# Kernel tuning notes

Hardware: AMD Instinct MI355X
Metric: run time of the kernel (lower is better)

## Reference

```python
import jax, jax.numpy as jnp
import numpy as np

DIM = 2048
N_HEADS = 32
N_KV_HEADS = 8
HEAD_DIM = 64
REPEATS = N_HEADS // N_KV_HEADS
SCALE = HEAD_DIM ** -0.5
L = 2048
B = 1


def rotary_matrix(context_len, d):
    # Dense (L, d, d) RoPE rotation matrix, exactly as get_rotary_matrix1.
    pos = jnp.arange(1, context_len + 1, dtype=jnp.float32)[:, None]
    i = jnp.arange(d // 2)
    theta = 10000.0 ** (-2.0 * i.astype(jnp.float32) / d)
    m_theta = pos * theta  # (L, d/2)
    cos_v, sin_v = jnp.cos(m_theta), jnp.sin(m_theta)
    R = jnp.zeros((context_len, d, d), dtype=jnp.float32)
    R = R.at[:, 2 * i, 2 * i].set(cos_v)
    R = R.at[:, 2 * i, 2 * i + 1].set(-sin_v)
    R = R.at[:, 2 * i + 1, 2 * i].set(sin_v)
    R = R.at[:, 2 * i + 1, 2 * i + 1].set(cos_v)
    return R


def causal_mask(context_len):
    idx = jnp.arange(context_len)
    return (idx[:, None] < idx[None, :]).astype(jnp.float32) * -1e9


def setup_inputs() -> dict:
    key = jax.random.key(0)
    ks = jax.random.split(key, 5)
    x = jax.random.normal(ks[0], (B, L, DIM), dtype=jnp.float32)
    mask = causal_mask(L)
    wq_w = jax.random.normal(ks[1], (N_HEADS * HEAD_DIM, DIM), dtype=jnp.float32) * 0.02
    wk_w = jax.random.normal(ks[2], (N_KV_HEADS * HEAD_DIM, DIM), dtype=jnp.float32) * 0.02
    wv_w = jax.random.normal(ks[3], (N_KV_HEADS * HEAD_DIM, DIM), dtype=jnp.float32) * 0.02
    wo_w = jax.random.normal(ks[4], (DIM, N_HEADS * HEAD_DIM), dtype=jnp.float32) * 0.02
    return {"x": x, "mask": mask, "wq_w": wq_w, "wk_w": wk_w, "wv_w": wv_w, "wo_w": wo_w}


def reference(x, mask, wq_w, wk_w, wv_w, wo_w):
    Bx, Lx, D = x.shape
    # projections (torch Linear: y = x @ W.T)
    q = jnp.einsum('bld,od->blo', x, wq_w).reshape(Bx, Lx, N_HEADS, HEAD_DIM).transpose(0, 2, 1, 3)
    k = jnp.einsum('bld,od->blo', x, wk_w).reshape(Bx, Lx, N_KV_HEADS, HEAD_DIM).transpose(0, 2, 1, 3)
    v = jnp.einsum('bld,od->blo', x, wv_w).reshape(Bx, Lx, N_KV_HEADS, HEAD_DIM).transpose(0, 2, 1, 3)
    # GQA repeat of kv heads (interleaved, matching concat-unsqueeze-reshape)
    k = jnp.repeat(k, REPEATS, axis=1)
    v = jnp.repeat(v, REPEATS, axis=1)
    # dense-matrix RoPE on q and (repeated) k
    R = rotary_matrix(Lx, HEAD_DIM)
    q = jnp.einsum('bhlj,lij->bhli', q, R)
    k = jnp.einsum('bhlj,lij->bhli', k, R)
    scores = jnp.einsum('bhld,bhmd->bhlm', q, k) * SCALE + mask
    attn = jax.nn.softmax(scores.astype(jnp.float32), axis=-1)
    out = jnp.einsum('bhlm,bhmd->bhld', attn, v)
    out = out.transpose(0, 2, 1, 3).reshape(Bx, Lx, N_HEADS * HEAD_DIM)
    out = jnp.einsum('blo,do->bld', out, wo_w)
    return out, k, v
```

## Files before the change

kernel.cpp:

```cpp
#include <hip/hip_runtime.h>

typedef __bf16 bf16;
typedef __bf16 bf16x8 __attribute__((ext_vector_type(8)));
typedef float floatx4 __attribute__((ext_vector_type(4)));
typedef float floatx16 __attribute__((ext_vector_type(16)));
typedef unsigned int uint;

#define MFMA16(a, b, c) __builtin_amdgcn_mfma_f32_16x16x32_bf16((a), (b), (c), 0, 0, 0)
#define MFMA32(a, b, c) __builtin_amdgcn_mfma_f32_32x32x16_bf16((a), (b), (c), 0, 0, 0)

__device__ __forceinline__ void gl2lds16(const bf16* g, bf16* l) {
  __builtin_amdgcn_global_load_lds(
      (const __attribute__((address_space(1))) void*)g,
      (__attribute__((address_space(3))) void*)l, 16, 0, 0);
}
__device__ __forceinline__ void wait_vm0() { __builtin_amdgcn_s_waitcnt(0x0f70); }

__device__ __forceinline__ void cvt8(const float* __restrict__ s,
                                     bf16* __restrict__ d, int i8) {
  const float4 a = ((const float4*)s)[i8 * 2];
  const float4 b = ((const float4*)s)[i8 * 2 + 1];
  bf16x8 o;
  o[0] = (bf16)a.x; o[1] = (bf16)a.y; o[2] = (bf16)a.z; o[3] = (bf16)a.w;
  o[4] = (bf16)b.x; o[5] = (bf16)b.y; o[6] = (bf16)b.z; o[7] = (bf16)b.w;
  *(bf16x8*)(d + i8 * 8) = o;
}

__global__ __launch_bounds__(256) void convert_kernel(
    const float* __restrict__ x, const float* __restrict__ wq,
    const float* __restrict__ wk, const float* __restrict__ wv,
    const float* __restrict__ wo, bf16* __restrict__ xb,
    bf16* __restrict__ wqb, bf16* __restrict__ wkb, bf16* __restrict__ wvb,
    bf16* __restrict__ wob) {
  const int g = blockIdx.x * 256 + threadIdx.x;
  if (g < 524288) cvt8(x, xb, g);
  else if (g < 1048576) cvt8(wq, wqb, g - 524288);
  else if (g < 1179648) cvt8(wk, wkb, g - 1048576);
  else if (g < 1310720) cvt8(wv, wvb, g - 1179648);
  else cvt8(wo, wob, g - 1310720);
}

template <typename OutT>
__device__ __forceinline__ void gemm_tile_body64(
    const bf16* __restrict__ A, int lda,
    const bf16* __restrict__ B, int ldb,
    OutT* __restrict__ C, int ldc, int K,
    bf16* S) {
  const int t = threadIdx.x;
  const int w = t >> 6, lane = t & 63;
  const int l15 = lane & 15, qd = lane >> 4;
  const int wr = w >> 1, wc = w & 1;

  floatx4 acc[2][4];
#pragma unroll
  for (int i = 0; i < 2; ++i)
#pragma unroll
    for (int j = 0; j < 4; ++j) acc[i][j] = (floatx4){0.f, 0.f, 0.f, 0.f};

  const bf16* gb[6];
  int lo[6];
#pragma unroll
  for (int i = 0; i < 6; ++i) {
    const int u = w + 4 * i;
    lo[i] = u * 512 + lane * 8;
    if (u < 8) {
      gb[i] = A + ((u >> 1) * 16 + l15) * lda + (u & 1) * 32 + qd * 8;
    } else {
      const int v = u - 8;
      gb[i] = B + ((v >> 1) * 16 + l15) * ldb + (v & 1) * 32 + qd * 8;
    }
  }

#define STG64(kt_, buf_)                                            \
  {                                                                 \
    bf16* d_ = S + (buf_) * 12288;                                  \
    _Pragma("unroll")                                               \
    for (int i_ = 0; i_ < 6; ++i_)                                  \
      gl2lds16(gb[i_] + (kt_) * 64, d_ + lo[i_]);                   \
  }

  const int NT = K >> 6;
  STG64(0, 0);
  wait_vm0();
  __syncthreads();
  int cur = 0;
  for (int kt = 0; kt < NT; ++kt) {
    if (kt + 1 < NT) STG64(kt + 1, cur ^ 1);
    const bf16* Ab = S + cur * 12288;
    const bf16* Bb = Ab + 4096;
    bf16x8 a[2][2], b[4][2];
#pragma unroll
    for (int i = 0; i < 2; ++i)
#pragma unroll
      for (int kk = 0; kk < 2; ++kk)
        a[i][kk] =
            *(const bf16x8*)(Ab + ((wr * 2 + i) * 2 + kk) * 512 + lane * 8);
#pragma unroll
    for (int j = 0; j < 4; ++j)
#pragma unroll
      for (int kk = 0; kk < 2; ++kk)
        b[j][kk] =
            *(const bf16x8*)(Bb + ((wc * 4 + j) * 2 + kk) * 512 + lane * 8);
#pragma unroll
    for (int kk = 0; kk < 2; ++kk)
#pragma unroll
      for (int i = 0; i < 2; ++i)
#pragma unroll
        for (int j = 0; j < 4; ++j)
          acc[i][j] = MFMA16(a[i][kk], b[j][kk], acc[i][j]);
    wait_vm0();
    __builtin_amdgcn_sched_barrier(0);
    __builtin_amdgcn_s_barrier();
    __builtin_amdgcn_sched_barrier(0);
    cur ^= 1;
  }
#undef STG64

#pragma unroll
  for (int i = 0; i < 2; ++i)
#pragma unroll
    for (int j = 0; j < 4; ++j) {
      const int row = wr * 32 + i * 16 + qd * 4;
      const int col = wc * 64 + j * 16 + l15;
#pragma unroll
      for (int r = 0; r < 4; ++r)
        C[(row + r) * ldc + col] = (OutT)acc[i][j][r];
    }
}

__global__ __launch_bounds__(256) void gemm_qkv(
    const bf16* __restrict__ x, const bf16* __restrict__ wq,
    const bf16* __restrict__ wk, const bf16* __restrict__ wv,
    bf16* __restrict__ Qws, bf16* __restrict__ Kh, bf16* __restrict__ Vh,
    bf16* __restrict__ Vt) {
  __shared__ bf16 As[4096], Bs[4096];
  const int bid = blockIdx.y * 24 + blockIdx.x;
  const int swz = (bid & 7) * 48 + (bid >> 3);
  const int nb = swz % 24;
  const int m0 = (swz / 24) * 128;
  const bf16* B;
  if (nb < 16) B = wq + nb * 128 * 2048;
  else if (nb < 20) B = wk + (nb - 16) * 128 * 2048;
  else B = wv + (nb - 20) * 128 * 2048;

  const int t = threadIdx.x;
  const int w = t >> 6, lane = t & 63;
  const int l15 = lane & 15, qd = lane >> 4;
  const int wr = w >> 1, wc = w & 1;

  floatx4 acc[4][4];
#pragma unroll
  for (int i = 0; i < 4; ++i)
#pragma unroll
    for (int j = 0; j < 4; ++j) acc[i][j] = (floatx4){0.f, 0.f, 0.f, 0.f};

  const bf16* A = x + m0 * 2048;
  const int mt0 = w, mt1 = w + 4;
  const int kseg = qd * 8;
  const bf16* ga0 = A + (mt0 * 16 + l15) * 2048 + kseg;
  const bf16* ga1 = A + (mt1 * 16 + l15) * 2048 + kseg;
  const bf16* gb0 = B + (mt0 * 16 + l15) * 2048 + kseg;
  const bf16* gb1 = B + (mt1 * 16 + l15) * 2048 + kseg;
  bf16* lA0 = As + mt0 * 512 + lane * 8;
  bf16* lA1 = As + mt1 * 512 + lane * 8;
  bf16* lB0 = Bs + mt0 * 512 + lane * 8;
  bf16* lB1 = Bs + mt1 * 512 + lane * 8;

  for (int k0 = 0; k0 < 2048; k0 += 32) {
    gl2lds16(ga0 + k0, lA0);
    gl2lds16(ga1 + k0, lA1);
    gl2lds16(gb0 + k0, lB0);
    gl2lds16(gb1 + k0, lB1);
    wait_vm0();
    __syncthreads();

    bf16x8 a[4], b[4];
#pragma unroll
    for (int i = 0; i < 4; ++i)
      a[i] = *(const bf16x8*)(As + (wr * 4 + i) * 512 + lane * 8);
#pragma unroll
    for (int j = 0; j < 4; ++j)
      b[j] = *(const bf16x8*)(Bs + (wc * 4 + j) * 512 + lane * 8);
#pragma unroll
    for (int i = 0; i < 4; ++i)
#pragma unroll
      for (int j = 0; j < 4; ++j) acc[i][j] = MFMA16(a[i], b[j], acc[i][j]);
    __syncthreads();
  }

  const float NEG_LOG2_10000_D32 = -0.4152410118609203f;
  const int odd = l15 & 1;
#pragma unroll
  for (int i = 0; i < 4; ++i)
#pragma unroll
    for (int j = 0; j < 4; ++j) {
      const int row = wr * 64 + i * 16 + qd * 4;
      const int col = wc * 64 + j * 16 + l15;
#pragma unroll
      for (int r = 0; r < 4; ++r) {
        const float own = acc[i][j][r];
        const int rg = m0 + row + r;
        if (nb < 16) {
          const float part = __shfl_xor(own, 1);
          const int gcol = nb * 128 + col;
          const int a = (gcol & 63) >> 1;
          const float ang =
              (float)(rg + 1) * exp2f(NEG_LOG2_10000_D32 * (float)a);
          float s, c;
          __sincosf(ang, &s, &c);
          const float val = odd ? (s * part + c * own) : (c * own - s * part);
          Qws[rg * 2048 + gcol] = (bf16)val;
        } else if (nb < 20) {
          const float part = __shfl_xor(own, 1);
          const int g512 = (nb - 16) * 128 + col;
          const int kvh = g512 >> 6, d = g512 & 63;
          const int a = d >> 1;
          const float ang =
              (float)(rg + 1) * exp2f(NEG_LOG2_10000_D32 * (float)a);
          float s, c;
          __sincosf(ang, &s, &c);
          const float val = odd ? (s * part + c * own) : (c * own - s * part);
          Kh[(kvh * 2048 + rg) * 64 + d] = (bf16)val;
        } else {
          const int g512 = (nb - 20) * 128 + col;
          const int kvh = g512 >> 6, d = g512 & 63;
          Vh[(kvh * 2048 + rg) * 64 + d] = (bf16)own;
          Vt[kvh * 131072 + d * 2048 + rg] = (bf16)own;
        }
      }
    }
}

__global__ __launch_bounds__(256) void gemm_o(
    const bf16* __restrict__ Ows, const bf16* __restrict__ wo,
    float* __restrict__ out) {
  __shared__ bf16 S[24576];
  const int bid = blockIdx.y * 16 + blockIdx.x;
  const int swz = (bid & 7) * 64 + (bid >> 3);
  const int n0 = (swz & 15) * 128;
  const int m0 = (swz >> 4) * 64;
  gemm_tile_body64<float>(Ows + m0 * 2048, 2048, wo + n0 * 2048, 2048,
                          out + m0 * 2048 + n0, 2048, 2048, S);
}

__global__ __launch_bounds__(256) void flash_kernel(
    const bf16* __restrict__ Qws, const bf16* __restrict__ Kh,
    const bf16* __restrict__ Vh, const bf16* __restrict__ Vt,
    bf16* __restrict__ Ows, float* __restrict__ Opart, float* __restrict__ ML,
    float* __restrict__ kout, float* __restrict__ vout) {
  __shared__ bf16 KVs[2][2][4096];
  __shared__ bf16 Osh[128 * 66];

  const int h = blockIdx.y;
  const int bx = blockIdx.x;
  int qt, seg, kts, kte;
  if (bx < 8) {
    qt = bx; seg = -1; kts = 0; kte = 2 * qt + 2;
  } else {
    const int i = bx - 8;
    qt = 8 + (i >> 1);
    seg = i & 1;
    const int half = qt + 1;
    kts = seg * half;
    kte = kts + half;
  }
  const int kh = h >> 2;
  const int q0 = qt * 128;
  const int t = threadIdx.x, w = t >> 6, lane = t & 63;
  const int l31 = lane & 31, hf = lane >> 5;
  const int qw = q0 + w * 32;

  const int s0 = w, s1 = w + 4;
  const bf16* gK0 = Kh + kh * 131072 + ((s0 >> 2) * 32 + l31) * 64 + (s0 & 3) * 16 + hf * 8;
  const bf16* gK1 = Kh + kh * 131072 + ((s1 >> 2) * 32 + l31) * 64 + (s1 & 3) * 16 + hf * 8;
  const bf16* gV0 = Vt + kh * 131072 + ((s0 >> 2) * 32 + l31) * 2048 + (s0 & 3) * 16 + hf * 8;
  const bf16* gV1 = Vt + kh * 131072 + ((s1 >> 2) * 32 + l31) * 2048 + (s1 & 3) * 16 + hf * 8;

  {
    const int nb = kts & 1;
    gl2lds16(gK0 + kts * 4096, &KVs[nb][0][s0 * 512 + lane * 8]);
    gl2lds16(gK1 + kts * 4096, &KVs[nb][0][s1 * 512 + lane * 8]);
    gl2lds16(gV0 + kts * 64, &KVs[nb][1][s0 * 512 + lane * 8]);
    gl2lds16(gV1 + kts * 64, &KVs[nb][1][s1 * 512 + lane * 8]);
  }

  bf16x8 qf[4];
  {
    const bf16* qrow = Qws + (qw + l31) * 2048 + h * 64 + hf * 8;
#pragma unroll
    for (int c = 0; c < 4; ++c) qf[c] = *(const bf16x8*)(qrow + c * 16);
  }

  {
    const int bid = (int)blockIdx.y * 24 + (int)blockIdx.x;
    for (uint u = (uint)(bid * 256 + t); u < 262144u; u += 196608u) {
      const uint u2 = u & 131071u;
      const bf16* src = (u < 131072u) ? Kh : Vh;
      float* dst = (u < 131072u) ? kout : vout;
      const int kvh2 = u2 >> 14;
      const int rr = u2 & 16383;
      const int l = rr >> 3, d8 = (rr & 7) * 8;
      const bf16x8 v = *(const bf16x8*)(src + (kvh2 * 2048 + l) * 64 + d8);
      float4 f0, f1;
      f0.x = (float)v[0]; f0.y = (float)v[1]; f0.z = (float)v[2]; f0.w = (float)v[3];
      f1.x = (float)v[4]; f1.y = (float)v[5]; f1.z = (float)v[6]; f1.w = (float)v[7];
#pragma unroll
      for (int rep = 0; rep < 4; ++rep) {
        float* o2 = dst + (((kvh2 * 4 + rep) * 2048 + l) * 64 + d8);
        *(float4*)o2 = f0;
        *(float4*)(o2 + 4) = f1;
      }
    }
  }

  floatx16 o[2] = {};
  float mrun = -3e38f, lrun = 0.f;

  const float C = 0.1803368801f;
  for (int kt = kts; kt < kte; ++kt) {
    wait_vm0();
    __syncthreads();
    if (kt + 1 < kte) {
      const int nb = (kt + 1) & 1;
      const int koff = (kt + 1) * 4096, voff = (kt + 1) * 64;
      gl2lds16(gK0 + koff, &KVs[nb][0][s0 * 512 + lane * 8]);
      gl2lds16(gK1 + koff, &KVs[nb][0][s1 * 512 + lane * 8]);
      gl2lds16(gV0 + voff, &KVs[nb][1][s0 * 512 + lane * 8]);
      gl2lds16(gV1 + voff, &KVs[nb][1][s1 * 512 + lane * 8]);
    }
    const int kt64 = kt * 64;
    if (kt64 > qw + 31) continue;
    const bf16* Kb = &KVs[kt & 1][0][0];
    const bf16* Vb = &KVs[kt & 1][1][0];

    floatx16 st[2];
    __builtin_amdgcn_s_setprio(1);
#pragma unroll
    for (int tt = 0; tt < 2; ++tt) {
      floatx16 z = {};
#pragma unroll
      for (int c = 0; c < 4; ++c) {
        const bf16x8 kf = *(const bf16x8*)(Kb + (tt * 4 + c) * 512 + lane * 8);
        z = MFMA32(kf, qf[c], z);
      }
      st[tt] = z;
    }
    __builtin_amdgcn_s_setprio(0);
    if (kt64 + 64 > qw) {
      const int myq = qw + l31;
#pragma unroll
      for (int tt = 0; tt < 2; ++tt)
#pragma unroll
        for (int r = 0; r < 16; ++r) {
          const int key = kt64 + tt * 32 + (r & 3) + 8 * (r >> 2) + 4 * hf;
          if (key > myq) st[tt][r] = -1e30f;
        }
    }
    float ma = -3e38f, mb = -3e38f, mc = -3e38f, md = -3e38f;
#pragma unroll
    for (int tt = 0; tt < 2; ++tt)
#pragma unroll
      for (int r = 0; r < 16; r += 4) {
        ma = fmaxf(ma, st[tt][r + 0]);
        mb = fmaxf(mb, st[tt][r + 1]);
        mc = fmaxf(mc, st[tt][r + 2]);
        md = fmaxf(md, st[tt][r + 3]);
      }
    float mx = fmaxf(fmaxf(ma, mb), fmaxf(mc, md));
    mx = fmaxf(mx, __shfl_xor(mx, 32));
    const bool defer = __all((mx - mrun) * C <= 8.f);
    if (!defer) {
      const float mn = fmaxf(mrun, mx);
      const float al = __builtin_amdgcn_exp2f((mrun - mn) * C);
      lrun *= al;
#pragma unroll
      for (int n = 0; n < 2; ++n)
#pragma unroll
        for (int r = 0; r < 16; ++r) o[n][r] *= al;
      mrun = mn;
    }
    float ra = 0.f, rb = 0.f, rc = 0.f, rd = 0.f;
#pragma unroll
    for (int tt = 0; tt < 2; ++tt)
#pragma unroll
      for (int r = 0; r < 16; r += 4) {
        const float p0 = __builtin_amdgcn_exp2f((st[tt][r + 0] - mrun) * C);
        const float p1 = __builtin_amdgcn_exp2f((st[tt][r + 1] - mrun) * C);
        const float p2 = __builtin_amdgcn_exp2f((st[tt][r + 2] - mrun) * C);
        const float p3 = __builtin_amdgcn_exp2f((st[tt][r + 3] - mrun) * C);
        st[tt][r + 0] = p0; ra += p0;
        st[tt][r + 1] = p1; rb += p1;
        st[tt][r + 2] = p2; rc += p2;
        st[tt][r + 3] = p3; rd += p3;
      }
    float rs = (ra + rb) + (rc + rd);
    rs += __shfl_xor(rs, 32);
    lrun += rs;

    uint pk[2][4][2];
#pragma unroll
    for (int tt = 0; tt < 2; ++tt)
#pragma unroll
      for (int g = 0; g < 4; ++g)
#pragma unroll
        for (int p = 0; p < 2; ++p) {
          union { bf16 h2[2]; uint u; } cv;
          cv.h2[0] = (bf16)st[tt][4 * g + 2 * p];
          cv.h2[1] = (bf16)st[tt][4 * g + 2 * p + 1];
          pk[tt][g][p] = cv.u;
        }
    uint own_[2][2][2], rv[2][2][2];
#pragma unroll
    for (int tt = 0; tt < 2; ++tt)
#pragma unroll
      for (int gam = 0; gam < 2; ++gam)
#pragma unroll
        for (int p = 0; p < 2; ++p) {
          own_[tt][gam][p] = hf ? pk[tt][2 * gam + 1][p] : pk[tt][2 * gam][p];
          const uint snd = hf ? pk[tt][2 * gam][p] : pk[tt][2 * gam + 1][p];
          rv[tt][gam][p] = (uint)__shfl_xor((int)snd, 32);
        }
    __builtin_amdgcn_s_setprio(1);
#pragma unroll
    for (int c = 0; c < 4; ++c) {
      const int tt = c >> 1, gam = c & 1;
      union { uint u[4]; bf16x8 v; } pf;
      pf.u[0] = hf ? rv[tt][gam][0] : own_[tt][gam][0];
      pf.u[1] = hf ? rv[tt][gam][1] : own_[tt][gam][1];
      pf.u[2] = hf ? own_[tt][gam][0] : rv[tt][gam][0];
      pf.u[3] = hf ? own_[tt][gam][1] : rv[tt][gam][1];
#pragma unroll
      for (int n = 0; n < 2; ++n)
        o[n] = MFMA32(*(const bf16x8*)(Vb + (n * 4 + c) * 512 + lane * 8),
                      pf.v, o[n]);
    }
    __builtin_amdgcn_s_setprio(0);
  }

  if (seg < 0) {
    const float inv = 1.f / lrun;
#pragma unroll
    for (int n = 0; n < 2; ++n)
#pragma unroll
      for (int r = 0; r < 16; ++r) {
        const int dl = n * 32 + (r & 3) + 8 * (r >> 2) + 4 * hf;
        Osh[(w * 32 + l31) * 66 + dl] = (bf16)(o[n][r] * inv);
      }
    __syncthreads();
#pragma unroll
    for (int i = 0; i < 4; ++i) {
      const int row = (t >> 3) + i * 32;
      const int col = (t & 7) * 8;
      const bf16x8 vv = *(const bf16x8*)&Osh[row * 66 + col];
      *(bf16x8*)&Ows[(q0 + row) * 2048 + h * 64 + col] = vv;
    }
  } else {
    const int idx = (h * 8 + (qt - 8)) * 2 + seg;
    float* Op = Opart + idx * 8192;
#pragma unroll
    for (int n = 0; n < 2; ++n)
#pragma unroll
      for (int r = 0; r < 16; ++r) {
        const int dl = n * 32 + (r & 3) + 8 * (r >> 2) + 4 * hf;
        Op[dl * 128 + w * 32 + l31] = o[n][r];
      }
    if (hf == 0) {
      ML[idx * 256 + w * 32 + l31] = mrun;
      ML[idx * 256 + 128 + w * 32 + l31] = lrun;
    }
  }
}

__global__ __launch_bounds__(256) void combine_kernel(
    const float* __restrict__ Opart, const float* __restrict__ ML,
    bf16* __restrict__ Ows) {
  __shared__ bf16 Osh[128 * 66];
  const int b = blockIdx.x;
  const int h = b >> 3, qt = (b & 7) + 8;
  const int q0 = qt * 128;
  const int t = threadIdx.x;
  const int row = t & 127, dh = t >> 7;
  const int i0 = (h * 8 + (qt - 8)) * 2;
  const float C = 0.1803368801f;
  const float m0 = ML[i0 * 256 + row], l0 = ML[i0 * 256 + 128 + row];
  const float m1 = ML[(i0 + 1) * 256 + row], l1 = ML[(i0 + 1) * 256 + 128 + row];
  const float m = fmaxf(m0, m1);
  const float w0 = __builtin_amdgcn_exp2f((m0 - m) * C);
  const float w1 = __builtin_amdgcn_exp2f((m1 - m) * C);
  const float inv = 1.f / (l0 * w0 + l1 * w1);
  const float* P0 = Opart + i0 * 8192;
  const float* P1 = Opart + (i0 + 1) * 8192;
#pragma unroll
  for (int j = 0; j < 32; ++j) {
    const int d = dh * 32 + j;
    const float v = (P0[d * 128 + row] * w0 + P1[d * 128 + row] * w1) * inv;
    Osh[row * 66 + d] = (bf16)v;
  }
  __syncthreads();
#pragma unroll
  for (int i = 0; i < 4; ++i) {
    const int r2 = (t >> 3) + i * 32;
    const int col = (t & 7) * 8;
    const bf16x8 vv = *(const bf16x8*)&Osh[r2 * 66 + col];
    *(bf16x8*)&Ows[(q0 + r2) * 2048 + h * 64 + col] = vv;
  }
}

extern "C" void kernel_launch(void* const* d_in, const int* in_sizes, int n_in,
                              void* d_out, int out_size, void* d_ws,
                              size_t ws_size, hipStream_t stream) {
  const float* x = (const float*)d_in[0];
  const float* wq = (const float*)d_in[2];
  const float* wk = (const float*)d_in[3];
  const float* wv = (const float*)d_in[4];
  const float* wo = (const float*)d_in[5];

  float* out = (float*)d_out;
  float* kout = out + 4194304;
  float* vout = out + 8388608;

  bf16* ws = (bf16*)d_ws;
  bf16* xb = ws;
  bf16* wqb = xb + 4194304;
  bf16* wkb = wqb + 4194304;
  bf16* wvb = wkb + 1048576;
  bf16* wob = wvb + 1048576;
  bf16* Qws = wob + 4194304;
  bf16* Kws = Qws + 4194304;
  bf16* Vh = Kws + 1048576;
  bf16* Vt = Vh + 1048576;
  bf16* Ows = Vt + 1048576;
  bf16* Kh = Ows + 4194304;
  float* Opart = out;
  float* MLf = (float*)Kws;

  convert_kernel<<<dim3(7168), dim3(256), 0, stream>>>(x, wq, wk, wv, wo, xb,
                                                       wqb, wkb, wvb, wob);
  gemm_qkv<<<dim3(24, 16), dim3(256), 0, stream>>>(xb, wqb, wkb, wvb, Qws, Kh,
                                                   Vh, Vt);
  flash_kernel<<<dim3(24, 32), dim3(256), 0, stream>>>(Qws, Kh, Vh, Vt, Ows,
                                                       Opart, MLf, kout, vout);
  combine_kernel<<<dim3(256), dim3(256), 0, stream>>>(Opart, MLf, Ows);
  gemm_o<<<dim3(16, 32), dim3(256), 0, stream>>>(Ows, wob, out);
}
```

Baseline: 290.3 us.

## Stage QKV epilogue through LDS for vector stores; load K/V directly in flash

The QKV GEMM epilogue now writes accumulators to a padded LDS tile, then applies RoPE on 8-wide vectors and issues 16-byte coalesced stores. The V transpose to Vt is done from LDS, replacing scattered 2-byte stores. The flash kernel drops its double-buffered LDS staging of K/V and loads fragments straight from global memory into registers per wave. Each wave now stops at its own causal limit, which removes block-wide barriers, but it risks exposed global load latency with no prefetch and redundant global reads across waves.

```diff
diff --git a/kernel.cpp b/kernel.cpp
--- a/kernel.cpp
+++ b/kernel.cpp
@@ -133,7 +133,9 @@
     const bf16* __restrict__ wk, const bf16* __restrict__ wv,
     bf16* __restrict__ Qws, bf16* __restrict__ Kh, bf16* __restrict__ Vh,
     bf16* __restrict__ Vt) {
-  __shared__ bf16 As[4096], Bs[4096];
+  __shared__ bf16 SM[17152];
+  bf16* As = SM;
+  bf16* Bs = SM + 4096;
   const int bid = blockIdx.y * 24 + blockIdx.x;
   const int swz = (bid & 7) * 48 + (bid >> 3);
   const int nb = swz % 24;
@@ -188,8 +190,6 @@
     __syncthreads();
   }
 
-  const float NEG_LOG2_10000_D32 = -0.4152410118609203f;
-  const int odd = l15 & 1;
 #pragma unroll
   for (int i = 0; i < 4; ++i)
 #pragma unroll
@@ -197,38 +197,74 @@
       const int row = wr * 64 + i * 16 + qd * 4;
       const int col = wc * 64 + j * 16 + l15;
 #pragma unroll
-      for (int r = 0; r < 4; ++r) {
-        const float own = acc[i][j][r];
-        const int rg = m0 + row + r;
-        if (nb < 16) {
-          const float part = __shfl_xor(own, 1);
-          const int gcol = nb * 128 + col;
-          const int a = (gcol & 63) >> 1;
-          const float ang =
-              (float)(rg + 1) * exp2f(NEG_LOG2_10000_D32 * (float)a);
-          float s, c;
-          __sincosf(ang, &s, &c);
-          const float val = odd ? (s * part + c * own) : (c * own - s * part);
-          Qws[rg * 2048 + gcol] = (bf16)val;
-        } else if (nb < 20) {
-          const float part = __shfl_xor(own, 1);
-          const int g512 = (nb - 16) * 128 + col;
-          const int kvh = g512 >> 6, d = g512 & 63;
-          const int a = d >> 1;
-          const float ang =
-              (float)(rg + 1) * exp2f(NEG_LOG2_10000_D32 * (float)a);
-          float s, c;
-          __sincosf(ang, &s, &c);
-          const float val = odd ? (s * part + c * own) : (c * own - s * part);
-          Kh[(kvh * 2048 + rg) * 64 + d] = (bf16)val;
-        } else {
-          const int g512 = (nb - 20) * 128 + col;
-          const int kvh = g512 >> 6, d = g512 & 63;
-          Vh[(kvh * 2048 + rg) * 64 + d] = (bf16)own;
-          Vt[kvh * 131072 + d * 2048 + rg] = (bf16)own;
-        }
-      }
-    }
+      for (int r = 0; r < 4; ++r)
+        SM[(row + r) * 134 + col] = (bf16)acc[i][j][r];
+    }
+  __syncthreads();
+
+  const float NEG_LOG2_10000_D32 = -0.4152410118609203f;
+  if (nb < 16) {
+#pragma unroll
+    for (int k = 0; k < 8; ++k) {
+      const int u = t + (k << 8);
+      const int row = u >> 4, c8 = (u & 15) << 3;
+      const bf16x8 v = *(const bf16x8*)&SM[row * 134 + c8];
+      const float base = (float)(m0 + row + 1);
+      bf16x8 ov;
+#pragma unroll
+      for (int p = 0; p < 4; ++p) {
+        const int a = ((c8 & 63) >> 1) + p;
+        float s, c;
+        __sincosf(base * exp2f(NEG_LOG2_10000_D32 * (float)a), &s, &c);
+        const float x0 = (float)v[2 * p], x1 = (float)v[2 * p + 1];
+        ov[2 * p] = (bf16)(c * x0 - s * x1);
+        ov[2 * p + 1] = (bf16)(s * x0 + c * x1);
+      }
+      *(bf16x8*)&Qws[(m0 + row) * 2048 + nb * 128 + c8] = ov;
+    }
+  } else if (nb < 20) {
+#pragma unroll
+    for (int k = 0; k < 8; ++k) {
+      const int u = t + (k << 8);
+      const int row = u >> 4, c8 = (u & 15) << 3;
+      const bf16x8 v = *(const bf16x8*)&SM[row * 134 + c8];
+      const float base = (float)(m0 + row + 1);
+      bf16x8 ov;
+#pragma unroll
+      for (int p = 0; p < 4; ++p) {
+        const int a = ((c8 & 63) >> 1) + p;
+        float s, c;
+        __sincosf(base * exp2f(NEG_LOG2_10000_D32 * (float)a), &s, &c);
+        const float x0 = (float)v[2 * p], x1 = (float)v[2 * p + 1];
+        ov[2 * p] = (bf16)(c * x0 - s * x1);
+        ov[2 * p + 1] = (bf16)(s * x0 + c * x1);
+      }
+      const int g512 = (nb - 16) * 128 + c8;
+      const int kvh = g512 >> 6, d8 = g512 & 63;
+      *(bf16x8*)&Kh[(kvh * 2048 + m0 + row) * 64 + d8] = ov;
+    }
+  } else {
+#pragma unroll
+    for (int k = 0; k < 8; ++k) {
+      const int u = t + (k << 8);
+      const int row = u >> 4, c8 = (u & 15) << 3;
+      const bf16x8 v = *(const bf16x8*)&SM[row * 134 + c8];
+      const int g512 = (nb - 20) * 128 + c8;
+      const int kvh = g512 >> 6, d8 = g512 & 63;
+      *(bf16x8*)&Vh[(kvh * 2048 + m0 + row) * 64 + d8] = v;
+    }
+#pragma unroll
+    for (int k = 0; k < 8; ++k) {
+      const int u = t + (k << 8);
+      const int col = u >> 4, r8 = (u & 15) << 3;
+      bf16x8 v;
+#pragma unroll
+      for (int jj = 0; jj < 8; ++jj) v[jj] = SM[(r8 + jj) * 134 + col];
+      const int g512 = (nb - 20) * 128 + col;
+      const int kvh = g512 >> 6, d = g512 & 63;
+      *(bf16x8*)&Vt[kvh * 131072 + d * 2048 + m0 + r8] = v;
+    }
+  }
 }
 
 __global__ __launch_bounds__(256) void gemm_o(
@@ -248,7 +284,6 @@
     const bf16* __restrict__ Vh, const bf16* __restrict__ Vt,
     bf16* __restrict__ Ows, float* __restrict__ Opart, float* __restrict__ ML,
     float* __restrict__ kout, float* __restrict__ vout) {
-  __shared__ bf16 KVs[2][2][4096];
   __shared__ bf16 Osh[128 * 66];
 
   const int h = blockIdx.y;
@@ -269,27 +304,6 @@
   const int t = threadIdx.x, w = t >> 6, lane = t & 63;
   const int l31 = lane & 31, hf = lane >> 5;
   const int qw = q0 + w * 32;
-
-  const int s0 = w, s1 = w + 4;
-  const bf16* gK0 = Kh + kh * 131072 + ((s0 >> 2) * 32 + l31) * 64 + (s0 & 3) * 16 + hf * 8;
-  const bf16* gK1 = Kh + kh * 131072 + ((s1 >> 2) * 32 + l31) * 64 + (s1 & 3) * 16 + hf * 8;
-  const bf16* gV0 = Vt + kh * 131072 + ((s0 >> 2) * 32 + l31) * 2048 + (s0 & 3) * 16 + hf * 8;
-  const bf16* gV1 = Vt + kh * 131072 + ((s1 >> 2) * 32 + l31) * 2048 + (s1 & 3) * 16 + hf * 8;
-
-  {
-    const int nb = kts & 1;
-    gl2lds16(gK0 + kts * 4096, &KVs[nb][0][s0 * 512 + lane * 8]);
-    gl2lds16(gK1 + kts * 4096, &KVs[nb][0][s1 * 512 + lane * 8]);
-    gl2lds16(gV0 + kts * 64, &KVs[nb][1][s0 * 512 + lane * 8]);
-    gl2lds16(gV1 + kts * 64, &KVs[nb][1][s1 * 512 + lane * 8]);
-  }
-
-  bf16x8 qf[4];
-  {
-    const bf16* qrow = Qws + (qw + l31) * 2048 + h * 64 + hf * 8;
-#pragma unroll
-    for (int c = 0; c < 4; ++c) qf[c] = *(const bf16x8*)(qrow + c * 16);
-  }
 
   {
     const int bid = (int)blockIdx.y * 24 + (int)blockIdx.x;
@@ -313,25 +327,32 @@
     }
   }
 
+  bf16x8 qf[4];
+  {
+    const bf16* qrow = Qws + (qw + l31) * 2048 + h * 64 + hf * 8;
+#pragma unroll
+    for (int c = 0; c < 4; ++c) qf[c] = *(const bf16x8*)(qrow + c * 16);
+  }
+
+  const bf16* kRow = Kh + kh * 131072 + l31 * 64 + hf * 8;
+  const bf16* vRow = Vt + kh * 131072 + l31 * 2048 + hf * 8;
+
   floatx16 o[2] = {};
   float mrun = -3e38f, lrun = 0.f;
 
+  const int kteW_ = ((qw + 31) >> 6) + 1;
+  const int kteW = kteW_ < kte ? kteW_ : kte;
+
   const float C = 0.1803368801f;
-  for (int kt = kts; kt < kte; ++kt) {
-    wait_vm0();
-    __syncthreads();
-    if (kt + 1 < kte) {
-      const int nb = (kt + 1) & 1;
-      const int koff = (kt + 1) * 4096, voff = (kt + 1) * 64;
-      gl2lds16(gK0 + koff, &KVs[nb][0][s0 * 512 + lane * 8]);
-      gl2lds16(gK1 + koff, &KVs[nb][0][s1 * 512 + lane * 8]);
-      gl2lds16(gV0 + voff, &KVs[nb][1][s0 * 512 + lane * 8]);
-      gl2lds16(gV1 + voff, &KVs[nb][1][s1 * 512 + lane * 8]);
-    }
+  for (int kt = kts; kt < kteW; ++kt) {
     const int kt64 = kt * 64;
-    if (kt64 > qw + 31) continue;
-    const bf16* Kb = &KVs[kt & 1][0][0];
-    const bf16* Vb = &KVs[kt & 1][1][0];
+
+    bf16x8 kf[2][4];
+#pragma unroll
+    for (int tt = 0; tt < 2; ++tt)
+#pragma unroll
+      for (int c = 0; c < 4; ++c)
+        kf[tt][c] = *(const bf16x8*)(kRow + (kt64 + tt * 32) * 64 + c * 16);
 
     floatx16 st[2];
     __builtin_amdgcn_s_setprio(1);
@@ -339,13 +360,18 @@
     for (int tt = 0; tt < 2; ++tt) {
       floatx16 z = {};
 #pragma unroll
-      for (int c = 0; c < 4; ++c) {
-        const bf16x8 kf = *(const bf16x8*)(Kb + (tt * 4 + c) * 512 + lane * 8);
-        z = MFMA32(kf, qf[c], z);
-      }
+      for (int c = 0; c < 4; ++c) z = MFMA32(kf[tt][c], qf[c], z);
       st[tt] = z;
     }
     __builtin_amdgcn_s_setprio(0);
+
+    bf16x8 vf[2][4];
+#pragma unroll
+    for (int n = 0; n < 2; ++n)
+#pragma unroll
+      for (int c = 0; c < 4; ++c)
+        vf[n][c] = *(const bf16x8*)(vRow + n * 65536 + kt64 + c * 16);
+
     if (kt64 + 64 > qw) {
       const int myq = qw + l31;
 #pragma unroll
@@ -430,9 +456,7 @@
       pf.u[2] = hf ? own_[tt][gam][0] : rv[tt][gam][0];
       pf.u[3] = hf ? own_[tt][gam][1] : rv[tt][gam][1];
 #pragma unroll
-      for (int n = 0; n < 2; ++n)
-        o[n] = MFMA32(*(const bf16x8*)(Vb + (n * 4 + c) * 512 + lane * 8),
-                      pf.v, o[n]);
+      for (int n = 0; n < 2; ++n) o[n] = MFMA32(vf[n][c], pf.v, o[n]);
     }
     __builtin_amdgcn_s_setprio(0);
   }
```

Measured after the change: 314.4 us. +8.3%, slower.
